# Optimization experiments

Measured on AMD Instinct MI355X. Metric: run time of the kernel, lower is better.

The kernel has to match this reference:

```python
import jax, jax.numpy as jnp
import numpy as np

B, T, C, H = 2, 2048, 1024, 16
HS = C // H                      # head_size = 64
LAYER_IDX = 2
LAMBDA_INIT = 0.8 - 0.6 * float(np.exp(-0.3 * (LAYER_IDX - 1)))
EPS = 1e-12


def setup_inputs() -> dict:
    key = jax.random.key(0)
    ks = jax.random.split(key, 22)
    std = 0.02
    w = lambda k, shape: (jax.random.normal(k, shape, jnp.float32) * std)
    inp = {
        'q': jax.random.normal(ks[0], (B, T, C), jnp.float32),
        'k': jax.random.normal(ks[1], (B, T, C), jnp.float32),
        'v': jax.random.normal(ks[2], (B, T, C), jnp.float32),
        'mask': jax.random.randint(ks[3], (B, T), 0, 2).astype(jnp.int32),
        # projection weights stored as (in, out) so y = x @ W + b
        'Wq1': w(ks[4], (C, C)), 'bq1': jnp.zeros((C,), jnp.float32),
        'Wq2': w(ks[5], (C, C)), 'bq2': jnp.zeros((C,), jnp.float32),
        'Wk1': w(ks[6], (C, C)), 'bk1': jnp.zeros((C,), jnp.float32),
        'Wk2': w(ks[7], (C, C)), 'bk2': jnp.zeros((C,), jnp.float32),
        'Wv':  w(ks[8], (C, 2 * C)), 'bv': jnp.zeros((2 * C,), jnp.float32),
        'Wc':  w(ks[9], (2 * C, C)), 'bc': jnp.zeros((C,), jnp.float32),
        'ln_w': jnp.ones((2 * HS,), jnp.float32),
        'ln_b': jnp.zeros((2 * HS,), jnp.float32),
        'lq1': jax.random.normal(ks[10], (H, HS), jnp.float32) * 0.1,
        'lk1': jax.random.normal(ks[11], (H, HS), jnp.float32) * 0.1,
        'lq2': jax.random.normal(ks[12], (H, HS), jnp.float32) * 0.1,
        'lk2': jax.random.normal(ks[13], (H, HS), jnp.float32) * 0.1,
    }
    return inp


def reference(q, k, v, mask, Wq1, bq1, Wq2, bq2, Wk1, bk1, Wk2, bk2,
              Wv, bv, Wc, bc, ln_w, ln_b, lq1, lk1, lq2, lk2):
    def heads(x, d):  # [B,T,H*d] -> [B,H,T,d]
        return x.reshape(B, T, H, d).transpose(0, 2, 1, 3)

    q1 = heads(q @ Wq1 + bq1, HS)
    q2 = heads(q @ Wq2 + bq2, HS)
    k1 = heads(k @ Wk1 + bk1, HS)
    k2 = heads(k @ Wk2 + bk2, HS)
    vv = heads(v @ Wv + bv, 2 * HS)          # [B,H,T,2*HS]

    scale = 1.0 / np.sqrt(HS)
    att1 = jnp.einsum('bhqd,bhkd->bhqk', q1, k1) * scale
    att2 = jnp.einsum('bhqd,bhkd->bhqk', q2, k2) * scale

    m = (mask == 0)[:, None, :, None]         # [B,1,Tq,1] -> masks query rows
    att1 = jnp.where(m, -1e9, att1)
    att2 = jnp.where(m, -1e9, att2)
    att1 = jax.nn.softmax(att1, axis=-1)
    att2 = jax.nn.softmax(att2, axis=-1)

    lam1 = jnp.exp(jnp.sum(lq1 * lk1, axis=-1))   # [H]
    lam2 = jnp.exp(jnp.sum(lq2 * lk2, axis=-1))
    lam = (lam1 - lam2 + LAMBDA_INIT)[None, :, None, None]
    att = att1 - lam * att2                       # differential attention

    y = jnp.einsum('bhqk,bhkd->bhqd', att, vv)    # [B,H,T,2*HS]

    # per-head TF-style LayerNorm over 2*HS, then (1 - lambda_init) scale
    u = y.mean(-1, keepdims=True)
    s = ((y - u) ** 2).mean(-1, keepdims=True)
    y = ln_w * ((y - u) / jnp.sqrt(s + EPS)) + ln_b
    y = y * (1.0 - LAMBDA_INIT)

    y = y.transpose(0, 2, 1, 3).reshape(B, T, 2 * C)
    return y @ Wc + bc
```

## Files before the change

kernel.cpp:

```cpp
#include <hip/hip_runtime.h>
#include <hip/hip_bf16.h>
#include <stdint.h>


#define T_SEQ 2048

typedef unsigned short u16;
typedef __attribute__((ext_vector_type(8))) short short8;
typedef __attribute__((ext_vector_type(4))) float f32x4;
typedef __attribute__((ext_vector_type(16))) float f32x16;

#define LAMBDA_INIT 0.35550906759096926f
#define ONE_MINUS_LI 0.6444909324090307f
#define SM_SCALE 0.125f
#define LOG2E 1.44269504f

__device__ __forceinline__ u16 f2bf(float f) {
  uint32_t u = __float_as_uint(f);
  return (u16)((u + 0x7FFFu + ((u >> 16) & 1u)) >> 16);
}
__device__ __forceinline__ float b2f(u16 u) {
  return __uint_as_float(((uint32_t)u) << 16);
}
__device__ __forceinline__ short8 ld8(const u16* p) {
  return *reinterpret_cast<const short8*>(p);
}
__device__ __forceinline__ void st8(u16* p, short8 v) {
  *reinterpret_cast<short8*>(p) = v;
}
__device__ __forceinline__ f32x4 mfma16(short8 a, short8 b, f32x4 c) {
  return __builtin_amdgcn_mfma_f32_16x16x32_bf16(a, b, c, 0, 0, 0);
}
__device__ __forceinline__ f32x16 mfma32(short8 a, short8 b, f32x16 c) {
  return __builtin_amdgcn_mfma_f32_32x32x16_bf16(a, b, c, 0, 0, 0);
}
__device__ __forceinline__ uint32_t cvtpk(float lo, float hi_) {
  uint32_t r;
  asm("v_cvt_pk_bf16_f32 %0, %1, %2" : "=v"(r) : "v"(lo), "v"(hi_));
  return r;
}

__global__ __launch_bounds__(256) void cvt_bf16(const float* __restrict__ in,
                                                u16* __restrict__ out, int n) {
  int i = (blockIdx.x * 256 + threadIdx.x) * 4;
  if (i >= n) return;
  float4 f = *reinterpret_cast<const float4*>(in + i);
  union { u16 u[4]; uint2 v; } pk;
  pk.u[0] = f2bf(f.x); pk.u[1] = f2bf(f.y); pk.u[2] = f2bf(f.z); pk.u[3] = f2bf(f.w);
  *reinterpret_cast<uint2*>(out + i) = pk.v;
}

__global__ __launch_bounds__(256) void tcvt(const float* __restrict__ W,
                                            u16* __restrict__ WT,
                                            int K, int N, int outRowOff) {
  __shared__ float tile[32][33];
  int n0 = blockIdx.x * 32, k0 = blockIdx.y * 32;
  int tx = threadIdx.x & 31, ty = threadIdx.x >> 5;
#pragma unroll
  for (int p = 0; p < 4; ++p)
    tile[ty + 8 * p][tx] = W[(size_t)(k0 + ty + 8 * p) * N + n0 + tx];
  __syncthreads();
#pragma unroll
  for (int p = 0; p < 4; ++p)
    WT[(size_t)(outRowOff + n0 + ty + 8 * p) * K + k0 + tx] = f2bf(tile[tx][ty + 8 * p]);
}

__global__ __launch_bounds__(256) void bias_concat(const float* __restrict__ b1,
                                                   const float* __restrict__ b2,
                                                   float* __restrict__ out) {
  int i = blockIdx.x * 256 + threadIdx.x;
  out[i] = (i < 1024) ? b1[i] : b2[i - 1024];
}

#define BM 128
#define BN 128
#define BK 64

template <int EPI>
__global__ __launch_bounds__(256) void gemm_bt(const u16* __restrict__ A,
                                               const u16* __restrict__ BT,
                                               const float* __restrict__ bias,
                                               void* __restrict__ Cv,
                                               int M, int N, int K) {
  __shared__ __align__(16) u16 As[BM * BK];
  __shared__ __align__(16) u16 Bs[BN * BK];
  int t = threadIdx.x;
  int w = t >> 6, l = t & 63;
  int g = l >> 4, c16 = l & 15;
  int wr = w >> 1, wc = w & 1;
  size_t gm = (size_t)blockIdx.y * BM, gn = (size_t)blockIdx.x * BN;

  f32x4 acc[4][4] = {};

  int srow = l >> 3;
  int scol = (l & 7) * 8;
  const u16* Ag = A + (gm + w * 32 + srow) * (size_t)K + scol;
  const u16* Bg = BT + (gn + w * 32 + srow) * (size_t)K + scol;

  for (int kt = 0; kt < K; kt += BK) {
    __syncthreads();
#pragma unroll
    for (int c = 0; c < 4; ++c) {
      __builtin_amdgcn_global_load_lds(
          (const __attribute__((address_space(1))) void*)(Ag + (size_t)(c * 8) * K + kt),
          (__attribute__((address_space(3))) void*)&As[(w * 32 + c * 8) * BK], 16, 0, 0);
      __builtin_amdgcn_global_load_lds(
          (const __attribute__((address_space(1))) void*)(Bg + (size_t)(c * 8) * K + kt),
          (__attribute__((address_space(3))) void*)&Bs[(w * 32 + c * 8) * BK], 16, 0, 0);
    }
    __syncthreads();
#pragma unroll
    for (int kk = 0; kk < 2; ++kk) {
      short8 af[4], bf[4];
#pragma unroll
      for (int m = 0; m < 4; ++m)
        af[m] = *reinterpret_cast<const short8*>(
            &As[(wr * 64 + m * 16 + c16) * BK + kk * 32 + g * 8]);
#pragma unroll
      for (int n = 0; n < 4; ++n)
        bf[n] = *reinterpret_cast<const short8*>(
            &Bs[(wc * 64 + n * 16 + c16) * BK + kk * 32 + g * 8]);
#pragma unroll
      for (int m = 0; m < 4; ++m)
#pragma unroll
        for (int n = 0; n < 4; ++n)
          acc[m][n] = mfma16(af[m], bf[n], acc[m][n]);
    }
  }

#pragma unroll
  for (int m = 0; m < 4; ++m)
#pragma unroll
    for (int n = 0; n < 4; ++n) {
      int row0 = (int)gm + wr * 64 + m * 16 + g * 4;
      int col = (int)gn + wc * 64 + n * 16 + c16;
      float bz = bias[col];
      if (EPI == 0) {
        u16* C = (u16*)Cv;
#pragma unroll
        for (int r = 0; r < 4; ++r)
          C[(size_t)(row0 + r) * N + col] = f2bf(acc[m][n][r] + bz);
      } else if (EPI == 1) {
        u16* C = (u16*)Cv;
        int bb = row0 >> 11, tt = row0 & 2047;
        union { u16 u[4]; uint2 v; } pk;
#pragma unroll
        for (int r = 0; r < 4; ++r) pk.u[r] = f2bf(acc[m][n][r] + bz);
        *reinterpret_cast<uint2*>(&C[((size_t)(bb * 2048 + col)) * 2048 + tt]) = pk.v;
      } else {
        float* C = (float*)Cv;
#pragma unroll
        for (int r = 0; r < 4; ++r)
          C[(size_t)(row0 + r) * N + col] = acc[m][n][r] + bz;
      }
    }
}

#define KROW 72
#define VROW 40
#define YROW 72
__global__ __launch_bounds__(256, 3) void diffattn(
    const u16* __restrict__ q1q2, const u16* __restrict__ k1k2,
    const u16* __restrict__ vvT, const int* __restrict__ mask,
    const float* __restrict__ lq1, const float* __restrict__ lk1,
    const float* __restrict__ lq2, const float* __restrict__ lk2,
    const float* __restrict__ lnw, const float* __restrict__ lnb,
    u16* __restrict__ yout) {
  __shared__ __align__(16) u16 smem[2][9728];

  int tid = threadIdx.x;
  int w = tid >> 6, l = tid & 63;
  int q = l & 31, hi = l >> 5;
  int pair = w >> 1, stream = w & 1;
  int bh = blockIdx.y, b = bh >> 4, h = bh & 15;
  int qr0 = blockIdx.x * 64 + pair * 32;

  float lm1 = lq1[h * 64 + l] * lk1[h * 64 + l];
  float lm2 = lq2[h * 64 + l] * lk2[h * 64 + l];
#pragma unroll
  for (int o = 32; o; o >>= 1) {
    lm1 += __shfl_xor(lm1, o);
    lm2 += __shfl_xor(lm2, o);
  }
  float lam = __expf(lm1) - __expf(lm2) + LAMBDA_INIT;

  int soff = stream * 1024;
  const u16* qrow = q1q2 + (size_t)(b * T_SEQ + qr0 + q) * 2048 + h * 64 + soff + hi * 8;
  short8 qf[4];
#pragma unroll
  for (int c = 0; c < 4; ++c) qf[c] = ld8(qrow + c * 16);

  float scale = (mask[b * T_SEQ + qr0 + q] == 0) ? 0.f : (SM_SCALE * LOG2E);

  float M = -INFINITY, L = 0.f;
  f32x16 acc[4] = {};

  int ku = tid * 2;
  int krow = ku >> 3, kslot = ku & 7;
  int kstream = krow >> 5, kkey = krow & 31;
  const u16* srcK = k1k2 + (size_t)(b * T_SEQ + kkey) * 2048 + h * 64 + kstream * 1024 + kslot * 8;
  int dK = (kstream * 32 + kkey) * KROW + kslot * 8;
  int vd = tid >> 1, vslot = (tid & 1) * 2;
  const u16* srcV = vvT + ((size_t)(b * 16 + h) * 128 + vd) * 2048 + vslot * 8;
  int dV = 4608 + vd * VROW + vslot * 8;

  {
    short8 k0 = ld8(srcK), k1v = ld8(srcK + 8);
    short8 v0 = ld8(srcV), v1 = ld8(srcV + 8);
    st8(&smem[0][dK], k0); st8(&smem[0][dK + 8], k1v);
    st8(&smem[0][dV], v0); st8(&smem[0][dV + 8], v1);
  }
  __syncthreads();

  short8 kr0, kr1, vr0, vr1;
  for (int kt = 0; kt < T_SEQ; kt += 32) {
    int cur = (kt >> 5) & 1;
    bool more = (kt + 32 < T_SEQ);
    if (more) {
      const u16* nk = srcK + (size_t)(kt + 32) * 2048;
      kr0 = ld8(nk); kr1 = ld8(nk + 8);
      const u16* nv = srcV + (kt + 32);
      vr0 = ld8(nv); vr1 = ld8(nv + 8);
    }

    const u16* Ksm = &smem[cur][0];
    const u16* Vsm = &smem[cur][4608];

    const u16* kbase = &Ksm[(stream * 32 + q) * KROW + hi * 8];
    short8 kf[4];
#pragma unroll
    for (int c = 0; c < 4; ++c) kf[c] = ld8(kbase + c * 16);

    f32x16 s = {};
#pragma unroll
    for (int c = 0; c < 4; ++c) s = mfma32(kf[c], qf[c], s);

    float x[16];
#pragma unroll
    for (int r = 0; r < 16; ++r) x[r] = s[r] * scale;

    float t8[8], t4[4];
#pragma unroll
    for (int i = 0; i < 8; ++i) t8[i] = fmaxf(x[i], x[i + 8]);
#pragma unroll
    for (int i = 0; i < 4; ++i) t4[i] = fmaxf(t8[i], t8[i + 4]);
    float tm = fmaxf(fmaxf(t4[0], t4[1]), fmaxf(t4[2], t4[3]));
    tm = fmaxf(tm, __shfl_xor(tm, 32));

    if (!__all(tm - M <= 11.5f)) {
      float Mn = fmaxf(M, tm);
      float a = exp2f(M - Mn);
      L *= a;
#pragma unroll
      for (int d = 0; d < 4; ++d) acc[d] *= a;
      M = Mn;
    }

    float p[16];
#pragma unroll
    for (int r = 0; r < 16; ++r) p[r] = exp2f(x[r] - M);
    float s8[8], s4[4];
#pragma unroll
    for (int i = 0; i < 8; ++i) s8[i] = p[i] + p[i + 8];
#pragma unroll
    for (int i = 0; i < 4; ++i) s4[i] = s8[i] + s8[i + 4];
    float ps = (s4[0] + s4[1]) + (s4[2] + s4[3]);
    ps += __shfl_xor(ps, 32);
    L += ps;

    uint32_t a1 = cvtpk(p[0], p[1]), a2 = cvtpk(p[2], p[3]);
    uint32_t b1 = cvtpk(p[4], p[5]), b2 = cvtpk(p[6], p[7]);
    uint32_t c1 = cvtpk(p[8], p[9]), c2 = cvtpk(p[10], p[11]);
    uint32_t d1 = cvtpk(p[12], p[13]), d2 = cvtpk(p[14], p[15]);
    uint32_t sa1 = (uint32_t)__shfl_xor((int)a1, 32), sa2 = (uint32_t)__shfl_xor((int)a2, 32);
    uint32_t sb1 = (uint32_t)__shfl_xor((int)b1, 32), sb2 = (uint32_t)__shfl_xor((int)b2, 32);
    uint32_t sc1 = (uint32_t)__shfl_xor((int)c1, 32), sc2 = (uint32_t)__shfl_xor((int)c2, 32);
    uint32_t sd1 = (uint32_t)__shfl_xor((int)d1, 32), sd2 = (uint32_t)__shfl_xor((int)d2, 32);
    union { uint32_t u[4]; short8 s8v; } pu0, pu1;
    pu0.u[0] = hi ? sb1 : a1;  pu0.u[1] = hi ? sb2 : a2;
    pu0.u[2] = hi ? b1 : sa1;  pu0.u[3] = hi ? b2 : sa2;
    pu1.u[0] = hi ? sd1 : c1;  pu1.u[1] = hi ? sd2 : c2;
    pu1.u[2] = hi ? d1 : sc1;  pu1.u[3] = hi ? d2 : sc2;
    short8 pf0 = pu0.s8v, pf1 = pu1.s8v;

#pragma unroll
    for (int d = 0; d < 4; ++d) {
      const u16* vb0 = &Vsm[(d * 32 + q) * VROW + hi * 8];
      short8 vf0 = ld8(vb0);
      short8 vf1 = ld8(vb0 + 16);
      acc[d] = mfma32(vf0, pf0, acc[d]);
      acc[d] = mfma32(vf1, pf1, acc[d]);
    }

    if (more) {
      u16* nb = &smem[cur ^ 1][0];
      st8(&nb[dK], kr0); st8(&nb[dK + 8], kr1);
      st8(&nb[dV], vr0); st8(&nb[dV + 8], vr1);
    }
    __syncthreads();
  }

  float inv = 1.f / L;
  u16* Ysm = &smem[0][0];
  if (stream == 1) {
    u16* yrow = &Ysm[(pair * 64 + l) * YROW];
#pragma unroll
    for (int d = 0; d < 4; ++d) {
      union { uint32_t u[8]; short8 v[2]; } pk;
#pragma unroll
      for (int i = 0; i < 8; ++i)
        pk.u[i] = cvtpk(acc[d][2 * i] * inv, acc[d][2 * i + 1] * inv);
      st8(yrow + d * 16, pk.v[0]);
      st8(yrow + d * 16 + 8, pk.v[1]);
    }
  }
  __syncthreads();
  if (stream == 0) {
    const u16* yrow = &Ysm[(pair * 64 + l) * YROW];
    float y[4][16];
#pragma unroll
    for (int d = 0; d < 4; ++d) {
      short8 y2a = ld8(yrow + d * 16);
      short8 y2b = ld8(yrow + d * 16 + 8);
#pragma unroll
      for (int i = 0; i < 8; ++i) {
        y[d][i] = acc[d][i] * inv - lam * b2f((u16)y2a[i]);
        y[d][8 + i] = acc[d][8 + i] * inv - lam * b2f((u16)y2b[i]);
      }
    }
    float sm = 0.f;
#pragma unroll
    for (int d = 0; d < 4; ++d)
#pragma unroll
      for (int r = 0; r < 16; ++r) sm += y[d][r];
    sm += __shfl_xor(sm, 32);
    float u = sm * (1.f / 128.f);
    float var = 0.f;
#pragma unroll
    for (int d = 0; d < 4; ++d)
#pragma unroll
      for (int r = 0; r < 16; ++r) { float dd = y[d][r] - u; var += dd * dd; }
    var += __shfl_xor(var, 32);
    float rstd = rsqrtf(var * (1.f / 128.f) + 1e-12f);

    size_t orow = (size_t)(b * T_SEQ + qr0 + q) * 2048 + h * 128;
#pragma unroll
    for (int d = 0; d < 4; ++d)
#pragma unroll
      for (int rr = 0; rr < 4; ++rr) {
        int base = d * 32 + 8 * rr + 4 * hi;
        union { u16 u[4]; uint2 v; } o;
#pragma unroll
        for (int i = 0; i < 4; ++i) {
          float yv = (lnw[base + i] * ((y[d][rr * 4 + i] - u) * rstd) + lnb[base + i]) *
                     ONE_MINUS_LI;
          o.u[i] = f2bf(yv);
        }
        *reinterpret_cast<uint2*>(&yout[orow + base]) = o.v;
      }
  }
}

extern "C" void kernel_launch(void* const* d_in, const int* in_sizes, int n_in,
                              void* d_out, int out_size, void* d_ws, size_t ws_size,
                              hipStream_t stream) {
  (void)in_sizes; (void)n_in; (void)out_size; (void)ws_size;
  const float* q   = (const float*)d_in[0];
  const float* k   = (const float*)d_in[1];
  const float* v   = (const float*)d_in[2];
  const int* maskp = (const int*)d_in[3];
  const float* Wq1 = (const float*)d_in[4];
  const float* bq1 = (const float*)d_in[5];
  const float* Wq2 = (const float*)d_in[6];
  const float* bq2 = (const float*)d_in[7];
  const float* Wk1 = (const float*)d_in[8];
  const float* bk1 = (const float*)d_in[9];
  const float* Wk2 = (const float*)d_in[10];
  const float* bk2 = (const float*)d_in[11];
  const float* Wv  = (const float*)d_in[12];
  const float* bv  = (const float*)d_in[13];
  const float* Wc  = (const float*)d_in[14];
  const float* bc  = (const float*)d_in[15];
  const float* lnw = (const float*)d_in[16];
  const float* lnb = (const float*)d_in[17];
  const float* lq1 = (const float*)d_in[18];
  const float* lk1 = (const float*)d_in[19];
  const float* lq2 = (const float*)d_in[20];
  const float* lk2 = (const float*)d_in[21];

  char* ws = (char*)d_ws;
  u16* qb     = (u16*)(ws + 0);
  u16* kb     = (u16*)(ws + 8388608);
  u16* vb     = (u16*)(ws + 16777216);
  u16* Wq12T  = (u16*)(ws + 25165824);
  u16* Wk12T  = (u16*)(ws + 29360128);
  u16* WvT    = (u16*)(ws + 33554432);
  u16* WcT    = (u16*)(ws + 37748736);
  float* biasq = (float*)(ws + 41943040);
  float* biask = (float*)(ws + 41951232);
  u16* q1q2   = (u16*)(ws + 41959424);
  u16* k1k2   = (u16*)(ws + 58736640);
  u16* vvT    = (u16*)(ws + 75513856);
  u16* yb     = (u16*)(ws + 0);

  const int NELEM = 2 * T_SEQ * 1024;

  cvt_bf16<<<4096, 256, 0, stream>>>(q, qb, NELEM);
  cvt_bf16<<<4096, 256, 0, stream>>>(k, kb, NELEM);
  cvt_bf16<<<4096, 256, 0, stream>>>(v, vb, NELEM);

  tcvt<<<dim3(32, 32), 256, 0, stream>>>(Wq1, Wq12T, 1024, 1024, 0);
  tcvt<<<dim3(32, 32), 256, 0, stream>>>(Wq2, Wq12T, 1024, 1024, 1024);
  tcvt<<<dim3(32, 32), 256, 0, stream>>>(Wk1, Wk12T, 1024, 1024, 0);
  tcvt<<<dim3(32, 32), 256, 0, stream>>>(Wk2, Wk12T, 1024, 1024, 1024);
  tcvt<<<dim3(64, 32), 256, 0, stream>>>(Wv, WvT, 1024, 2048, 0);
  tcvt<<<dim3(32, 64), 256, 0, stream>>>(Wc, WcT, 2048, 1024, 0);

  bias_concat<<<8, 256, 0, stream>>>(bq1, bq2, biasq);
  bias_concat<<<8, 256, 0, stream>>>(bk1, bk2, biask);

  gemm_bt<0><<<dim3(16, 32), 256, 0, stream>>>(qb, Wq12T, biasq, q1q2, 4096, 2048, 1024);
  gemm_bt<0><<<dim3(16, 32), 256, 0, stream>>>(kb, Wk12T, biask, k1k2, 4096, 2048, 1024);
  gemm_bt<1><<<dim3(16, 32), 256, 0, stream>>>(vb, WvT, bv, vvT, 4096, 2048, 1024);

  diffattn<<<dim3(32, 32), 256, 0, stream>>>(q1q2, k1k2, vvT, maskp,
                                             lq1, lk1, lq2, lk2, lnw, lnb, yb);

  gemm_bt<2><<<dim3(8, 32), 256, 0, stream>>>(yb, WcT, bc, d_out, 4096, 1024, 2048);
}
```

Before: 345.6 us.

## Single-buffer attention LDS, remap grid for head locality, scale after max

Drops the LDS double buffer in the differential attention kernel, halving shared memory per block, and stages K/V in registers with two barriers per key tile. The launch becomes a 1D grid remapped so that consecutive blocks cover 8 heads across query tiles, which is meant to improve L2 reuse of K/V. The row max is now taken on raw scores and scaled once, and the exponent uses a single fma. The intent is higher occupancy and less VALU work, at the cost of an extra barrier per iteration and less overlap between LDS stores and compute.

Result: faster. 330.0 us (-4.5%).

```diff
diff --git a/kernel.cpp b/kernel.cpp
--- a/kernel.cpp
+++ b/kernel.cpp
@@ -166,14 +166,22 @@
     const float* __restrict__ lq2, const float* __restrict__ lk2,
     const float* __restrict__ lnw, const float* __restrict__ lnb,
     u16* __restrict__ yout) {
-  __shared__ __align__(16) u16 smem[2][9728];
+  __shared__ __align__(16) u16 smem[9728];
+  u16* Ksm = smem;
+  u16* Vsm = smem + 4608;
+  u16* Ysm = smem;
 
   int tid = threadIdx.x;
   int w = tid >> 6, l = tid & 63;
   int q = l & 31, hi = l >> 5;
   int pair = w >> 1, stream = w & 1;
-  int bh = blockIdx.y, b = bh >> 4, h = bh & 15;
-  int qr0 = blockIdx.x * 64 + pair * 32;
+
+  int id = blockIdx.x;
+  int j = id & 7, rest = id >> 3;
+  int xblk = rest & 31, ygrp = rest >> 5;
+  int bh = ygrp * 8 + j;
+  int b = bh >> 4, h = bh & 15;
+  int qr0 = xblk * 64 + pair * 32;
 
   float lm1 = lq1[h * 64 + l] * lk1[h * 64 + l];
   float lm2 = lq2[h * 64 + l] * lk2[h * 64 + l];
@@ -199,33 +207,26 @@
   int krow = ku >> 3, kslot = ku & 7;
   int kstream = krow >> 5, kkey = krow & 31;
   const u16* srcK = k1k2 + (size_t)(b * T_SEQ + kkey) * 2048 + h * 64 + kstream * 1024 + kslot * 8;
-  int dK = (kstream * 32 + kkey) * KROW + kslot * 8;
+  u16* dstK = &Ksm[(kstream * 32 + kkey) * KROW + kslot * 8];
   int vd = tid >> 1, vslot = (tid & 1) * 2;
   const u16* srcV = vvT + ((size_t)(b * 16 + h) * 128 + vd) * 2048 + vslot * 8;
-  int dV = 4608 + vd * VROW + vslot * 8;
-
-  {
-    short8 k0 = ld8(srcK), k1v = ld8(srcK + 8);
-    short8 v0 = ld8(srcV), v1 = ld8(srcV + 8);
-    st8(&smem[0][dK], k0); st8(&smem[0][dK + 8], k1v);
-    st8(&smem[0][dV], v0); st8(&smem[0][dV + 8], v1);
-  }
-  __syncthreads();
-
-  short8 kr0, kr1, vr0, vr1;
+  u16* dstV = &Vsm[vd * VROW + vslot * 8];
+
+  short8 kr0 = ld8(srcK), kr1 = ld8(srcK + 8);
+  short8 vr0 = ld8(srcV), vr1 = ld8(srcV + 8);
+
   for (int kt = 0; kt < T_SEQ; kt += 32) {
-    int cur = (kt >> 5) & 1;
-    bool more = (kt + 32 < T_SEQ);
-    if (more) {
+    __syncthreads();
+    st8(dstK, kr0); st8(dstK + 8, kr1);
+    st8(dstV, vr0); st8(dstV + 8, vr1);
+    __syncthreads();
+    if (kt + 32 < T_SEQ) {
       const u16* nk = srcK + (size_t)(kt + 32) * 2048;
       kr0 = ld8(nk); kr1 = ld8(nk + 8);
       const u16* nv = srcV + (kt + 32);
       vr0 = ld8(nv); vr1 = ld8(nv + 8);
     }
 
-    const u16* Ksm = &smem[cur][0];
-    const u16* Vsm = &smem[cur][4608];
-
     const u16* kbase = &Ksm[(stream * 32 + q) * KROW + hi * 8];
     short8 kf[4];
 #pragma unroll
@@ -235,17 +236,16 @@
 #pragma unroll
     for (int c = 0; c < 4; ++c) s = mfma32(kf[c], qf[c], s);
 
-    float x[16];
-#pragma unroll
-    for (int r = 0; r < 16; ++r) x[r] = s[r] * scale;
-
-    float t8[8], t4[4];
-#pragma unroll
-    for (int i = 0; i < 8; ++i) t8[i] = fmaxf(x[i], x[i + 8]);
-#pragma unroll
-    for (int i = 0; i < 4; ++i) t4[i] = fmaxf(t8[i], t8[i + 4]);
-    float tm = fmaxf(fmaxf(t4[0], t4[1]), fmaxf(t4[2], t4[3]));
-    tm = fmaxf(tm, __shfl_xor(tm, 32));
+    float rm = fmaxf(fmaxf(s[0], s[1]), s[2]);
+    rm = fmaxf(fmaxf(rm, s[3]), s[4]);
+    rm = fmaxf(fmaxf(rm, s[5]), s[6]);
+    rm = fmaxf(fmaxf(rm, s[7]), s[8]);
+    rm = fmaxf(fmaxf(rm, s[9]), s[10]);
+    rm = fmaxf(fmaxf(rm, s[11]), s[12]);
+    rm = fmaxf(fmaxf(rm, s[13]), s[14]);
+    rm = fmaxf(rm, s[15]);
+    rm = fmaxf(rm, __shfl_xor(rm, 32));
+    float tm = rm * scale;
 
     if (!__all(tm - M <= 11.5f)) {
       float Mn = fmaxf(M, tm);
@@ -258,7 +258,7 @@
 
     float p[16];
 #pragma unroll
-    for (int r = 0; r < 16; ++r) p[r] = exp2f(x[r] - M);
+    for (int r = 0; r < 16; ++r) p[r] = exp2f(__builtin_fmaf(s[r], scale, -M));
     float s8[8], s4[4];
 #pragma unroll
     for (int i = 0; i < 8; ++i) s8[i] = p[i] + p[i + 8];
@@ -291,17 +291,10 @@
       acc[d] = mfma32(vf0, pf0, acc[d]);
       acc[d] = mfma32(vf1, pf1, acc[d]);
     }
-
-    if (more) {
-      u16* nb = &smem[cur ^ 1][0];
-      st8(&nb[dK], kr0); st8(&nb[dK + 8], kr1);
-      st8(&nb[dV], vr0); st8(&nb[dV + 8], vr1);
-    }
-    __syncthreads();
   }
 
   float inv = 1.f / L;
-  u16* Ysm = &smem[0][0];
+  __syncthreads();
   if (stream == 1) {
     u16* yrow = &Ysm[(pair * 64 + l) * YROW];
 #pragma unroll
@@ -423,8 +416,8 @@
   gemm_bt<0><<<dim3(16, 32), 256, 0, stream>>>(kb, Wk12T, biask, k1k2, 4096, 2048, 1024);
   gemm_bt<1><<<dim3(16, 32), 256, 0, stream>>>(vb, WvT, bv, vvT, 4096, 2048, 1024);
 
-  diffattn<<<dim3(32, 32), 256, 0, stream>>>(q1q2, k1k2, vvT, maskp,
-                                             lq1, lk1, lq2, lk2, lnw, lnb, yb);
+  diffattn<<<1024, 256, 0, stream>>>(q1q2, k1k2, vvT, maskp,
+                                     lq1, lk1, lq2, lk2, lnw, lnb, yb);
 
   gemm_bt<2><<<dim3(8, 32), 256, 0, stream>>>(yb, WcT, bc, d_out, 4096, 1024, 2048);
 }
```
